# Kernel optimization log

Hardware: AMD Instinct MI355X
Metric: run time of the kernel (lower is better)

The kernel has to match this reference:

```python
import jax, jax.numpy as jnp
import numpy as np

D_MODEL = 256
NHEAD = 8
DK = D_MODEL // NHEAD
EDGE_FEAT_DIM = 7
N_NODES = 2048
N_EDGES = 65536
LN_EPS = 1e-5


def _ln(x, g, b):
    mu = jnp.mean(x, axis=-1, keepdims=True)
    var = jnp.mean(jnp.square(x - mu), axis=-1, keepdims=True)
    return (x - mu) * jax.lax.rsqrt(var + LN_EPS) * g + b


def setup_inputs() -> dict:
    key = jax.random.key(0)
    ks = jax.random.split(key, 16)
    d, h2 = D_MODEL, 2 * D_MODEL
    s = 0.02
    inp = {
        "h": jax.random.normal(ks[0], (N_NODES, d), jnp.float32),
        "edge_attr": jax.random.normal(ks[1], (N_EDGES, EDGE_FEAT_DIM), jnp.float32),
        # weights stored as (in, out): y = x @ W + b (matches torch Linear math)
        "Wq": s * jax.random.normal(ks[2], (d, d), jnp.float32),
        "bq": jnp.zeros((d,), jnp.float32),
        "Wk": s * jax.random.normal(ks[3], (d, d), jnp.float32),
        "bk": jnp.zeros((d,), jnp.float32),
        "Wv": s * jax.random.normal(ks[4], (d, d), jnp.float32),
        "bv": jnp.zeros((d,), jnp.float32),
        "Wo": s * jax.random.normal(ks[5], (d, d), jnp.float32),
        "bo": jnp.zeros((d,), jnp.float32),
        "We": s * jax.random.normal(ks[6], (EDGE_FEAT_DIM, NHEAD), jnp.float32),
        "be": jnp.zeros((NHEAD,), jnp.float32),
        "ln1_g": jnp.ones((d,), jnp.float32),
        "ln1_b": jnp.zeros((d,), jnp.float32),
        "fln_g": jnp.ones((d,), jnp.float32),
        "fln_b": jnp.zeros((d,), jnp.float32),
        "W1": s * jax.random.normal(ks[7], (d, h2), jnp.float32),
        "b1": jnp.zeros((h2,), jnp.float32),
        "W2": s * jax.random.normal(ks[8], (h2, d), jnp.float32),
        "b2": jnp.zeros((d,), jnp.float32),
        "edge_index": jax.random.randint(ks[9], (2, N_EDGES), 0, N_NODES, jnp.int64 if jax.config.jax_enable_x64 else jnp.int32),
    }
    return inp


def reference(h, edge_attr, Wq, bq, Wk, bk, Wv, bv, Wo, bo, We, be,
              ln1_g, ln1_b, fln_g, fln_b, W1, b1, W2, b2, edge_index):
    N = h.shape[0]
    res = h
    # edge bias scattered into dense (N, N, H) tensor
    eb = edge_attr @ We + be                                  # (E, H)
    attn_bias = jnp.zeros((N, N, NHEAD), h.dtype).at[edge_index[0], edge_index[1]].set(eb)
    Q = (h @ Wq + bq).reshape(N, NHEAD, DK)
    K = (h @ Wk + bk).reshape(N, NHEAD, DK)
    V = (h @ Wv + bv).reshape(N, NHEAD, DK)
    scores = jnp.einsum('nhd,mhd->nmh', Q, K) / jnp.sqrt(jnp.float32(DK)) + attn_bias
    attn = jax.nn.softmax(scores, axis=1)                     # softmax over keys m
    out = jnp.einsum('nmh,mhd->nhd', attn, V).reshape(N, D_MODEL)
    out = out @ Wo + bo
    h1 = _ln(res + out, ln1_g, ln1_b)
    ffn = jax.nn.gelu(_ln(h1, fln_g, fln_b) @ W1 + b1, approximate=False) @ W2 + b2
    return h1 + ffn
```

## Files before the change

### kernel.cpp

```cpp
#include <hip/hip_runtime.h>
#include <math.h>

#define NN 2048
#define NE 65536
#define DM 256
#define NH 8
#define DKH 32
#define CAP 128
#define TM2 128
#define SPLIT 4

typedef __attribute__((ext_vector_type(8))) short bf16x8;
typedef __attribute__((ext_vector_type(4))) float f32x4;

#define WAVE_LDS_SYNC() __asm__ volatile("s_waitcnt lgkmcnt(0)" ::: "memory")

__device__ __forceinline__ unsigned short f2b(float f) {
    unsigned u = __float_as_uint(f);
    unsigned r = (u + 0x7FFFu + ((u >> 16) & 1u)) >> 16;
    return (unsigned short)r;
}
__device__ __forceinline__ float b2f(unsigned short s) {
    return __uint_as_float(((unsigned)s) << 16);
}
__device__ __forceinline__ unsigned pk2(float a, float b) {
    unsigned ua = __float_as_uint(a) + 0x8000u;
    unsigned ub = __float_as_uint(b) + 0x8000u;
    return (ua >> 16) | (ub & 0xFFFF0000u);
}

__global__ __launch_bounds__(256) void prep_all_kernel(
    const float* __restrict__ Wq, const float* __restrict__ Wk,
    const float* __restrict__ Wv, const float* __restrict__ Wo,
    const float* __restrict__ W1, const float* __restrict__ W2,
    const float* __restrict__ ea, const float* __restrict__ We,
    const float* __restrict__ be, const int* __restrict__ ei,
    unsigned short* __restrict__ Wqkvt, unsigned short* __restrict__ Wot,
    unsigned short* __restrict__ W1t, unsigned short* __restrict__ W2t,
    float* __restrict__ eb, int* __restrict__ cnt, int* __restrict__ lst)
{
    int b = blockIdx.x;
    if (b < 2048) {
        int i = b * 256 + threadIdx.x;
        if (i < 196608) {
            int n = i >> 8, k = i & 255;
            const float* W = (n < 256) ? Wq : (n < 512) ? Wk : Wv;
            Wqkvt[i] = f2b(W[k * 256 + (n & 255)]);
        } else if (i < 262144) {
            int j = i - 196608;
            int n = j >> 8, k = j & 255;
            Wot[j] = f2b(Wo[k * 256 + n]);
        } else if (i < 393216) {
            int j = i - 262144;
            int n = j >> 8, k = j & 255;
            W1t[j] = f2b(W1[(size_t)k * 512 + n]);
        } else {
            int j = i - 393216;
            int n = j >> 9, k = j & 511;
            W2t[j] = f2b(W2[(size_t)k * 256 + n]);
        }
    } else {
        int e = (b - 2048) * 256 + threadIdx.x;
        float acc[NH];
#pragma unroll
        for (int hh = 0; hh < NH; ++hh) acc[hh] = be[hh];
#pragma unroll
        for (int f = 0; f < 7; ++f) {
            float x = ea[e * 7 + f];
#pragma unroll
            for (int hh = 0; hh < NH; ++hh) acc[hh] = fmaf(x, We[f * NH + hh], acc[hh]);
        }
#pragma unroll
        for (int hh = 0; hh < NH; ++hh)
            eb[e * NH + hh] = acc[hh] * 1.44269504088896f;
        int s = ei[e];
        int p = atomicAdd(&cnt[s], 1);
        if (p < CAP) lst[s * CAP + p] = e;
    }
}

__global__ __launch_bounds__(128) void rowprep_kernel(
    const int* __restrict__ ei, const int* __restrict__ cnt,
    const int* __restrict__ lst, int* __restrict__ sortedDest,
    int* __restrict__ sortedE, int* __restrict__ rowOff)
{
    __shared__ int ds[CAP], es[CAP];
    __shared__ int bc[16], off[17];
    int n = blockIdx.x, t = threadIdx.x;
    int c = cnt[n]; if (c > CAP) c = CAP;
    if (t < 16) bc[t] = 0;
    int e = -1, d = -1;
    if (t < c) { e = lst[n * CAP + t]; d = ei[NE + e]; }
    ds[t] = d; es[t] = e;
    __syncthreads();
    bool win = (t < c);
    if (win) {
        for (int j = 0; j < c; ++j)
            if (ds[j] == d && es[j] > e) { win = false; break; }
    }
    int bkt = (d >= 0) ? (d >> 7) : 0;
    int pos = -1;
    if (win) pos = atomicAdd(&bc[bkt], 1);
    __syncthreads();
    if (t == 0) {
        int s = 0;
        for (int i = 0; i < 16; ++i) { off[i] = s; s += bc[i]; }
        off[16] = s;
    }
    __syncthreads();
    if (win) {
        int p = off[bkt] + pos;
        sortedDest[n * CAP + p] = d;
        sortedE[n * CAP + p] = e;
    }
    if (t < 17) rowOff[n * 17 + t] = off[t];
}

template <int EPI, int MT, int AF32>
__global__ __launch_bounds__(MT * 4) void gemm_bf16(
    const void* __restrict__ Av, const unsigned short* __restrict__ Bt,
    const float* __restrict__ bias0, const float* __restrict__ bias1,
    const float* __restrict__ bias2, const float* __restrict__ resid,
    void* __restrict__ out0, void* __restrict__ out1, void* __restrict__ out2,
    int M, int N, int K)
{
    __shared__ __align__(16) unsigned short As[MT][136];
    __shared__ __align__(16) unsigned short Bs[64][136];
    int tid = threadIdx.x;
    int wv = tid >> 6, l = tid & 63, l15 = l & 15, quad = l >> 4;
    int m0 = blockIdx.y * MT, n0 = blockIdx.x * 64;

    f32x4 acc[4];
#pragma unroll
    for (int i = 0; i < 4; ++i) acc[i] = (f32x4){0.f, 0.f, 0.f, 0.f};

    for (int k0 = 0; k0 < K; k0 += 128) {
        if (MT == 64) {
            int row = tid >> 2, cb = (tid & 3) * 32;
            if (AF32) {
                const float* ap = (const float*)Av + (size_t)(m0 + row) * K + k0 + cb;
#pragma unroll
                for (int i = 0; i < 4; ++i) {
                    float4 f0 = *(const float4*)(ap + i * 8);
                    float4 f1 = *(const float4*)(ap + i * 8 + 4);
                    uint4 pk = { pk2(f0.x, f0.y), pk2(f0.z, f0.w),
                                 pk2(f1.x, f1.y), pk2(f1.z, f1.w) };
                    *(uint4*)&As[row][cb + i * 8] = pk;
                }
            } else {
                const unsigned short* ap =
                    (const unsigned short*)Av + (size_t)(m0 + row) * K + k0 + cb;
#pragma unroll
                for (int i = 0; i < 4; ++i)
                    *(uint4*)&As[row][cb + i * 8] = *(const uint4*)(ap + i * 8);
            }
            const unsigned short* bp = Bt + (size_t)(n0 + row) * K + k0 + cb;
#pragma unroll
            for (int i = 0; i < 4; ++i)
                *(uint4*)&Bs[row][cb + i * 8] = *(const uint4*)(bp + i * 8);
        } else {
            int rowa = tid >> 2, cba = (tid & 3) * 32;
            const unsigned short* ap =
                (const unsigned short*)Av + (size_t)(m0 + rowa) * K + k0 + cba;
#pragma unroll
            for (int i = 0; i < 4; ++i)
                *(uint4*)&As[rowa][cba + i * 8] = *(const uint4*)(ap + i * 8);
            int rowb = tid >> 1, cbb = (tid & 1) * 64;
            const unsigned short* bp = Bt + (size_t)(n0 + rowb) * K + k0 + cbb;
#pragma unroll
            for (int i = 0; i < 8; ++i)
                *(uint4*)&Bs[rowb][cbb + i * 8] = *(const uint4*)(bp + i * 8);
        }
        __syncthreads();
#pragma unroll
        for (int ks = 0; ks < 4; ++ks) {
            bf16x8 a = *(const bf16x8*)&As[wv * 16 + l15][ks * 32 + quad * 8];
#pragma unroll
            for (int nt = 0; nt < 4; ++nt) {
                bf16x8 b = *(const bf16x8*)&Bs[nt * 16 + l15][ks * 32 + quad * 8];
                acc[nt] = __builtin_amdgcn_mfma_f32_16x16x32_bf16(a, b, acc[nt], 0, 0, 0);
            }
        }
        __syncthreads();
    }

#pragma unroll
    for (int nt = 0; nt < 4; ++nt) {
        int colb = n0 + nt * 16;
        if (EPI == 2 && colb >= 512) {
            int n = colb + l15 - 512;
            float bv = bias2[n];
            uint2 pk = { pk2(acc[nt][0] + bv, acc[nt][1] + bv),
                         pk2(acc[nt][2] + bv, acc[nt][3] + bv) };
            *(uint2*)((unsigned short*)out2 + (size_t)n * NN + m0 + wv * 16 + quad * 4) = pk;
            continue;
        }
#pragma unroll
        for (int r = 0; r < 4; ++r) {
            int row = m0 + wv * 16 + quad * 4 + r;
            int col = colb + l15;
            float v = acc[nt][r];
            if (EPI == 0) {
                v += bias0[col];
                if (resid) v += resid[(size_t)row * N + col];
                ((float*)out0)[(size_t)row * N + col] = v;
            } else if (EPI == 1) {
                v += bias0[col];
                v = 0.5f * v * (1.0f + erff(v * 0.70710678118654752f));
                ((unsigned short*)out0)[(size_t)row * N + col] = f2b(v);
            } else {
                if (col < 256) {
                    v = (v + bias0[col]) * 0.2550348592f;
                    ((unsigned short*)out0)[(size_t)row * 256 + col] = f2b(v);
                } else {
                    v += bias1[col - 256];
                    ((unsigned short*)out1)[(size_t)row * 256 + col - 256] = f2b(v);
                }
            }
        }
    }
}

__global__ __launch_bounds__(256) void attn_mfma(
    const unsigned short* __restrict__ Qb, const unsigned short* __restrict__ Kb,
    const unsigned short* __restrict__ Vt, const float* __restrict__ eb,
    const int* __restrict__ sortedDest, const int* __restrict__ sortedE,
    const int* __restrict__ rowOff,
    float* __restrict__ accD, float* __restrict__ lD)
{
    __shared__ __align__(16) unsigned short Ks[TM2][40];
    __shared__ __align__(16) unsigned short Vs[32][TM2 + 8];
    __shared__ __align__(16) unsigned short Pn[4][16][TM2 + 16];
    int h = blockIdx.y, tid = threadIdx.x;
    int wv = tid >> 6, l = tid & 63, l15 = l & 15, quad = l >> 4;
    int n0 = blockIdx.x * 64 + wv * 16;
    int mz = blockIdx.z;

    bf16x8 aq = *(const bf16x8*)(Qb + (size_t)(n0 + l15) * DM + h * 32 + quad * 8);

    f32x4 oacc[2];
    oacc[0] = (f32x4){0.f, 0.f, 0.f, 0.f};
    oacc[1] = (f32x4){0.f, 0.f, 0.f, 0.f};
    float lacc = 0.f;
    float dreg = 0.f;
    const unsigned short* Vth = Vt + (size_t)h * 32 * NN;

    int r16 = l >> 2, sub = l & 3;
    int frow = n0 + r16;

    for (int t = 0; t < NN / (TM2 * SPLIT); ++t) {
        int m0 = (mz * (NN / SPLIT)) + t * TM2;
        int ti = m0 >> 7;
        {
            int r = tid >> 1, kc = (tid & 1) * 16;
            const unsigned short* ks = Kb + (size_t)(m0 + r) * DM + h * 32 + kc;
            *(uint4*)&Ks[r][kc]     = *(const uint4*)(ks);
            *(uint4*)&Ks[r][kc + 8] = *(const uint4*)(ks + 8);
            int d = tid >> 3, mc = (tid & 7) * 16;
            const unsigned short* vs = Vth + (size_t)d * NN + m0 + mc;
            *(uint4*)&Vs[d][mc]     = *(const uint4*)(vs);
            *(uint4*)&Vs[d][mc + 8] = *(const uint4*)(vs + 8);
        }
        __syncthreads();
#pragma unroll
        for (int mt = 0; mt < TM2 / 16; ++mt) {
            bf16x8 ak = *(const bf16x8*)&Ks[mt * 16 + l15][quad * 8];
            f32x4 s = __builtin_amdgcn_mfma_f32_16x16x32_bf16(
                ak, aq, (f32x4){0.f, 0.f, 0.f, 0.f}, 0, 0, 0);
            float p0 = __builtin_amdgcn_exp2f(s[0]);
            float p1 = __builtin_amdgcn_exp2f(s[1]);
            float p2 = __builtin_amdgcn_exp2f(s[2]);
            float p3 = __builtin_amdgcn_exp2f(s[3]);
            lacc += (p0 + p1) + (p2 + p3);
            *(uint2*)&Pn[wv][l15][mt * 16 + quad * 4] =
                (uint2){pk2(p0, p1), pk2(p2, p3)};
        }
        WAVE_LDS_SYNC();
        {
            int o0 = rowOff[frow * 17 + ti];
            int o1 = rowOff[frow * 17 + ti + 1];
            for (int idx = o0 + sub; idx < o1; idx += 4) {
                int d = sortedDest[frow * CAP + idx] - m0;
                int e = sortedE[frow * CAP + idx];
                float expb = __builtin_amdgcn_exp2f(eb[e * NH + h]);
                float pold = b2f(Pn[wv][r16][d]);
                Pn[wv][r16][d] = f2b(pold * expb);
                dreg += pold * (expb - 1.0f);
            }
        }
        WAVE_LDS_SYNC();
#pragma unroll
        for (int kc = 0; kc < TM2 / 32; ++kc) {
            bf16x8 ap = *(const bf16x8*)&Pn[wv][l15][kc * 32 + quad * 8];
#pragma unroll
            for (int nt = 0; nt < 2; ++nt) {
                bf16x8 bv = *(const bf16x8*)&Vs[nt * 16 + l15][kc * 32 + quad * 8];
                oacc[nt] = __builtin_amdgcn_mfma_f32_16x16x32_bf16(ap, bv, oacc[nt], 0, 0, 0);
            }
        }
        __syncthreads();
    }

    lacc += __shfl_xor(lacc, 16);
    lacc += __shfl_xor(lacc, 32);
    dreg += __shfl_xor(dreg, 1);
    dreg += __shfl_xor(dreg, 2);
    float dtot = __shfl(dreg, l15 * 4);
    float* lDp = lD + (size_t)mz * NN * NH;
    if (l < 16)
        lDp[(size_t)(n0 + l) * NH + h] = lacc + dtot;
    float* aDp = accD + (size_t)mz * NN * DM;
#pragma unroll
    for (int nt = 0; nt < 2; ++nt)
#pragma unroll
        for (int r = 0; r < 4; ++r)
            aDp[(size_t)(n0 + quad * 4 + r) * DM + h * 32 + nt * 16 + l15] = oacc[nt][r];
}

__global__ __launch_bounds__(256) void wo_ln_kernel(
    const float* __restrict__ accD, const float* __restrict__ lD,
    const unsigned short* __restrict__ Wot, const float* __restrict__ bo,
    const float* __restrict__ h, const float* __restrict__ g1,
    const float* __restrict__ b1, const float* __restrict__ g2,
    const float* __restrict__ b2, float* __restrict__ H1,
    unsigned short* __restrict__ X2b)
{
    __shared__ float linv[16][8];
    __shared__ __align__(16) unsigned short As[16][264];
    __shared__ __align__(16) unsigned short Bs[256][40];
    __shared__ float Tt[16][264];
    __shared__ unsigned short X2s[16][264];
    int tid = threadIdx.x, m0 = blockIdx.x * 16;
    int wv = tid >> 6, l = tid & 63, l15 = l & 15, quad = l >> 4;

    if (tid < 128) {
        int r = tid >> 3, hh = tid & 7;
        float ls = 0.f;
#pragma unroll
        for (int s = 0; s < SPLIT; ++s)
            ls += lD[(size_t)s * NN * NH + (size_t)(m0 + r) * NH + hh];
        linv[r][hh] = 1.0f / ls;
    }
    __syncthreads();
#pragma unroll
    for (int ch = 0; ch < 16; ++ch) {
        float o = 0.f;
#pragma unroll
        for (int s = 0; s < SPLIT; ++s)
            o += accD[(size_t)s * NN * DM + (size_t)(m0 + ch) * DM + tid];
        As[ch][tid] = f2b(o * linv[ch][tid >> 5]);
    }
    __syncthreads();

    f32x4 acc[4];
#pragma unroll
    for (int i = 0; i < 4; ++i) acc[i] = (f32x4){0.f, 0.f, 0.f, 0.f};

    for (int k0 = 0; k0 < 256; k0 += 32) {
#pragma unroll
        for (int ps = 0; ps < 4; ++ps) {
            int row = ps * 64 + (tid >> 2), kk = (tid & 3) * 8;
            *(uint4*)&Bs[row][kk] = *(const uint4*)(Wot + (size_t)row * 256 + k0 + kk);
        }
        __syncthreads();
        bf16x8 a = *(const bf16x8*)&As[l15][k0 + quad * 8];
#pragma unroll
        for (int nt = 0; nt < 4; ++nt) {
            bf16x8 b = *(const bf16x8*)&Bs[wv * 64 + nt * 16 + l15][quad * 8];
            acc[nt] = __builtin_amdgcn_mfma_f32_16x16x32_bf16(a, b, acc[nt], 0, 0, 0);
        }
        __syncthreads();
    }

#pragma unroll
    for (int nt = 0; nt < 4; ++nt)
#pragma unroll
        for (int r = 0; r < 4; ++r) {
            int row = quad * 4 + r, col = wv * 64 + nt * 16 + l15;
            Tt[row][col] = acc[nt][r] + bo[col] + h[(size_t)(m0 + row) * DM + col];
        }
    __syncthreads();

    int rr = tid >> 4, l16 = tid & 15;
    float x[16];
#pragma unroll
    for (int j = 0; j < 16; ++j) x[j] = Tt[rr][l16 + 16 * j];
    float mu = 0.f;
#pragma unroll
    for (int j = 0; j < 16; ++j) mu += x[j];
#pragma unroll
    for (int off = 1; off < 16; off <<= 1) mu += __shfl_xor(mu, off);
    mu *= (1.0f / 256.0f);
    float var = 0.f;
#pragma unroll
    for (int j = 0; j < 16; ++j) { float d = x[j] - mu; var += d * d; }
#pragma unroll
    for (int off = 1; off < 16; off <<= 1) var += __shfl_xor(var, off);
    float rs = rsqrtf(var * (1.0f / 256.0f) + 1e-5f);
    float y[16]; float mu2 = 0.f;
#pragma unroll
    for (int j = 0; j < 16; ++j) {
        int c = l16 + 16 * j;
        y[j] = (x[j] - mu) * rs * g1[c] + b1[c];
        mu2 += y[j];
    }
#pragma unroll
    for (int off = 1; off < 16; off <<= 1) mu2 += __shfl_xor(mu2, off);
    mu2 *= (1.0f / 256.0f);
    float var2 = 0.f;
#pragma unroll
    for (int j = 0; j < 16; ++j) { float d = y[j] - mu2; var2 += d * d; }
#pragma unroll
    for (int off = 1; off < 16; off <<= 1) var2 += __shfl_xor(var2, off);
    float rs2 = rsqrtf(var2 * (1.0f / 256.0f) + 1e-5f);
#pragma unroll
    for (int j = 0; j < 16; ++j) {
        int c = l16 + 16 * j;
        Tt[rr][c] = y[j];
        X2s[rr][c] = f2b((y[j] - mu2) * rs2 * g2[c] + b2[c]);
    }
    __syncthreads();
#pragma unroll
    for (int ch = 0; ch < 16; ++ch) {
        H1[(size_t)(m0 + ch) * DM + tid] = Tt[ch][tid];
        X2b[(size_t)(m0 + ch) * DM + tid] = X2s[ch][tid];
    }
}

extern "C" void kernel_launch(void* const* d_in, const int* in_sizes, int n_in,
                              void* d_out, int out_size, void* d_ws, size_t ws_size,
                              hipStream_t stream)
{
    const float* h    = (const float*)d_in[0];
    const float* ea   = (const float*)d_in[1];
    const float* Wq   = (const float*)d_in[2];
    const float* bq   = (const float*)d_in[3];
    const float* Wk   = (const float*)d_in[4];
    const float* bk   = (const float*)d_in[5];
    const float* Wv   = (const float*)d_in[6];
    const float* bv   = (const float*)d_in[7];
    const float* Wo   = (const float*)d_in[8];
    const float* bo   = (const float*)d_in[9];
    const float* We   = (const float*)d_in[10];
    const float* be   = (const float*)d_in[11];
    const float* ln1g = (const float*)d_in[12];
    const float* ln1b = (const float*)d_in[13];
    const float* flng = (const float*)d_in[14];
    const float* flnb = (const float*)d_in[15];
    const float* W1   = (const float*)d_in[16];
    const float* b1   = (const float*)d_in[17];
    const float* W2   = (const float*)d_in[18];
    const float* b2   = (const float*)d_in[19];
    const int*   ei   = (const int*)d_in[20];
    float* out = (float*)d_out;

    char* p = (char*)d_ws;
    float* eb   = (float*)p;           p += (size_t)NE * NH * 4;
    int*   cnt  = (int*)p;             p += (size_t)NN * 4;
    int*   lst  = (int*)p;             p += (size_t)NN * CAP * 4;
    int*   sD   = (int*)p;             p += (size_t)NN * CAP * 4;
    int*   sE   = (int*)p;             p += (size_t)NN * CAP * 4;
    int*   rOff = (int*)p;             p += (size_t)NN * 17 * 4;
    unsigned short* Wqkvt = (unsigned short*)p; p += (size_t)768 * 256 * 2;
    unsigned short* Wot   = (unsigned short*)p; p += (size_t)256 * 256 * 2;
    unsigned short* W1t   = (unsigned short*)p; p += (size_t)512 * 256 * 2;
    unsigned short* W2t   = (unsigned short*)p; p += (size_t)256 * 512 * 2;
    unsigned short* Qb    = (unsigned short*)p; p += (size_t)NN * DM * 2;
    unsigned short* Kb    = (unsigned short*)p; p += (size_t)NN * DM * 2;
    unsigned short* Vt    = (unsigned short*)p; p += (size_t)NN * DM * 2;
    float* accD = (float*)p;           p += (size_t)SPLIT * NN * DM * 4;
    float* lD   = (float*)p;           p += (size_t)SPLIT * NN * NH * 4;
    float* H1   = (float*)p;           p += (size_t)NN * DM * 4;
    unsigned short* X2b   = (unsigned short*)p; p += (size_t)NN * DM * 2;
    unsigned short* F1b   = (unsigned short*)p; p += (size_t)NN * 512 * 2;

    hipMemsetAsync(cnt, 0, (size_t)NN * 4, stream);
    prep_all_kernel<<<2048 + NE / 256, 256, 0, stream>>>(
        Wq, Wk, Wv, Wo, W1, W2, ea, We, be, ei,
        Wqkvt, Wot, W1t, W2t, eb, cnt, lst);
    rowprep_kernel<<<NN, 128, 0, stream>>>(ei, cnt, lst, sD, sE, rOff);

    gemm_bf16<2, 64, 1><<<dim3(768 / 64, NN / 64), 256, 0, stream>>>(
        h, Wqkvt, bq, bk, bv, nullptr, Qb, Kb, Vt, NN, 768, 256);

    attn_mfma<<<dim3(NN / 64, NH, SPLIT), 256, 0, stream>>>(
        Qb, Kb, Vt, eb, sD, sE, rOff, accD, lD);

    wo_ln_kernel<<<NN / 16, 256, 0, stream>>>(
        accD, lD, Wot, bo, h, ln1g, ln1b, flng, flnb, H1, X2b);

    gemm_bf16<1, 64, 0><<<dim3(512 / 64, NN / 64), 256, 0, stream>>>(
        X2b, W1t, b1, nullptr, nullptr, nullptr, F1b, nullptr, nullptr, NN, 512, 256);
    gemm_bf16<0, 32, 0><<<dim3(256 / 64, NN / 32), 128, 0, stream>>>(
        F1b, W2t, b2, nullptr, nullptr, H1, out, nullptr, nullptr, NN, 256, 512);
}
```

Before: 173.3 us.

## Fuse Wo projection, layernorms and both FFN GEMMs into one tail kernel

Merges the Wo+LN kernel with the two FFN GEMMs into a single kernel per 16-row block. H1, normalized X2 and GELU activations stay in shared memory rather than round-tripping through global buffers, and two launches go away. The cost is that each block reloads the full W1 and W2 weights from global/L2 with only 128 blocks, and each GEMM uses a single 16-row MFMA tile. Occupancy drops from the larger LDS footprint, so the FFN GEMMs may lose parallelism compared with the separate tiled kernels.

```diff
diff --git a/kernel.cpp b/kernel.cpp
--- a/kernel.cpp
+++ b/kernel.cpp
@@ -317,19 +317,22 @@
             aDp[(size_t)(n0 + quad * 4 + r) * DM + h * 32 + nt * 16 + l15] = oacc[nt][r];
 }
 
-__global__ __launch_bounds__(256) void wo_ln_kernel(
+__global__ __launch_bounds__(256) void tail_fused_kernel(
     const float* __restrict__ accD, const float* __restrict__ lD,
     const unsigned short* __restrict__ Wot, const float* __restrict__ bo,
-    const float* __restrict__ h, const float* __restrict__ g1,
-    const float* __restrict__ b1, const float* __restrict__ g2,
-    const float* __restrict__ b2, float* __restrict__ H1,
-    unsigned short* __restrict__ X2b)
+    const float* __restrict__ h, const float* __restrict__ ln1g,
+    const float* __restrict__ ln1b, const float* __restrict__ flng,
+    const float* __restrict__ flnb,
+    const unsigned short* __restrict__ W1t, const float* __restrict__ fb1,
+    const unsigned short* __restrict__ W2t, const float* __restrict__ fb2,
+    float* __restrict__ out)
 {
     __shared__ float linv[16][8];
     __shared__ __align__(16) unsigned short As[16][264];
-    __shared__ __align__(16) unsigned short Bs[256][40];
+    __shared__ __align__(16) unsigned short Wfs[512][40];
     __shared__ float Tt[16][264];
-    __shared__ unsigned short X2s[16][264];
+    __shared__ __align__(16) unsigned short X2s[16][264];
+    __shared__ __align__(16) unsigned short F1s[16][520];
     int tid = threadIdx.x, m0 = blockIdx.x * 16;
     int wv = tid >> 6, l = tid & 63, l15 = l & 15, quad = l >> 4;
 
@@ -360,13 +363,13 @@
 #pragma unroll
         for (int ps = 0; ps < 4; ++ps) {
             int row = ps * 64 + (tid >> 2), kk = (tid & 3) * 8;
-            *(uint4*)&Bs[row][kk] = *(const uint4*)(Wot + (size_t)row * 256 + k0 + kk);
+            *(uint4*)&Wfs[row][kk] = *(const uint4*)(Wot + (size_t)row * 256 + k0 + kk);
         }
         __syncthreads();
         bf16x8 a = *(const bf16x8*)&As[l15][k0 + quad * 8];
 #pragma unroll
         for (int nt = 0; nt < 4; ++nt) {
-            bf16x8 b = *(const bf16x8*)&Bs[wv * 64 + nt * 16 + l15][quad * 8];
+            bf16x8 b = *(const bf16x8*)&Wfs[wv * 64 + nt * 16 + l15][quad * 8];
             acc[nt] = __builtin_amdgcn_mfma_f32_16x16x32_bf16(a, b, acc[nt], 0, 0, 0);
         }
         __syncthreads();
@@ -401,7 +404,7 @@
 #pragma unroll
     for (int j = 0; j < 16; ++j) {
         int c = l16 + 16 * j;
-        y[j] = (x[j] - mu) * rs * g1[c] + b1[c];
+        y[j] = (x[j] - mu) * rs * ln1g[c] + ln1b[c];
         mu2 += y[j];
     }
 #pragma unroll
@@ -417,14 +420,65 @@
     for (int j = 0; j < 16; ++j) {
         int c = l16 + 16 * j;
         Tt[rr][c] = y[j];
-        X2s[rr][c] = f2b((y[j] - mu2) * rs2 * g2[c] + b2[c]);
-    }
-    __syncthreads();
-#pragma unroll
-    for (int ch = 0; ch < 16; ++ch) {
-        H1[(size_t)(m0 + ch) * DM + tid] = Tt[ch][tid];
-        X2b[(size_t)(m0 + ch) * DM + tid] = X2s[ch][tid];
-    }
+        X2s[rr][c] = f2b((y[j] - mu2) * rs2 * flng[c] + flnb[c]);
+    }
+    __syncthreads();
+
+    f32x4 acc1[8];
+#pragma unroll
+    for (int i = 0; i < 8; ++i) acc1[i] = (f32x4){0.f, 0.f, 0.f, 0.f};
+
+    for (int k0 = 0; k0 < 256; k0 += 32) {
+#pragma unroll
+        for (int ps = 0; ps < 8; ++ps) {
+            int row = ps * 64 + (tid >> 2), kk = (tid & 3) * 8;
+            *(uint4*)&Wfs[row][kk] = *(const uint4*)(W1t + (size_t)row * 256 + k0 + kk);
+        }
+        __syncthreads();
+        bf16x8 a = *(const bf16x8*)&X2s[l15][k0 + quad * 8];
+#pragma unroll
+        for (int nt = 0; nt < 8; ++nt) {
+            bf16x8 b = *(const bf16x8*)&Wfs[wv * 128 + nt * 16 + l15][quad * 8];
+            acc1[nt] = __builtin_amdgcn_mfma_f32_16x16x32_bf16(a, b, acc1[nt], 0, 0, 0);
+        }
+        __syncthreads();
+    }
+#pragma unroll
+    for (int nt = 0; nt < 8; ++nt)
+#pragma unroll
+        for (int r = 0; r < 4; ++r) {
+            int row = quad * 4 + r, col = wv * 128 + nt * 16 + l15;
+            float v = acc1[nt][r] + fb1[col];
+            v = 0.5f * v * (1.0f + erff(v * 0.70710678118654752f));
+            F1s[row][col] = f2b(v);
+        }
+
+    f32x4 acc2[4];
+#pragma unroll
+    for (int i = 0; i < 4; ++i) acc2[i] = (f32x4){0.f, 0.f, 0.f, 0.f};
+
+    for (int k0 = 0; k0 < 512; k0 += 32) {
+#pragma unroll
+        for (int ps = 0; ps < 4; ++ps) {
+            int row = ps * 64 + (tid >> 2), kk = (tid & 3) * 8;
+            *(uint4*)&Wfs[row][kk] = *(const uint4*)(W2t + (size_t)row * 512 + k0 + kk);
+        }
+        __syncthreads();
+        bf16x8 a = *(const bf16x8*)&F1s[l15][k0 + quad * 8];
+#pragma unroll
+        for (int nt = 0; nt < 4; ++nt) {
+            bf16x8 b = *(const bf16x8*)&Wfs[wv * 64 + nt * 16 + l15][quad * 8];
+            acc2[nt] = __builtin_amdgcn_mfma_f32_16x16x32_bf16(a, b, acc2[nt], 0, 0, 0);
+        }
+        __syncthreads();
+    }
+#pragma unroll
+    for (int nt = 0; nt < 4; ++nt)
+#pragma unroll
+        for (int r = 0; r < 4; ++r) {
+            int row = quad * 4 + r, col = wv * 64 + nt * 16 + l15;
+            out[(size_t)(m0 + row) * DM + col] = acc2[nt][r] + fb2[col] + Tt[row][col];
+        }
 }
 
 extern "C" void kernel_launch(void* const* d_in, const int* in_sizes, int n_in,
@@ -470,9 +524,6 @@
     unsigned short* Vt    = (unsigned short*)p; p += (size_t)NN * DM * 2;
     float* accD = (float*)p;           p += (size_t)SPLIT * NN * DM * 4;
     float* lD   = (float*)p;           p += (size_t)SPLIT * NN * NH * 4;
-    float* H1   = (float*)p;           p += (size_t)NN * DM * 4;
-    unsigned short* X2b   = (unsigned short*)p; p += (size_t)NN * DM * 2;
-    unsigned short* F1b   = (unsigned short*)p; p += (size_t)NN * 512 * 2;
 
     hipMemsetAsync(cnt, 0, (size_t)NN * 4, stream);
     prep_all_kernel<<<2048 + NE / 256, 256, 0, stream>>>(
@@ -486,11 +537,7 @@
     attn_mfma<<<dim3(NN / 64, NH, SPLIT), 256, 0, stream>>>(
         Qb, Kb, Vt, eb, sD, sE, rOff, accD, lD);
 
-    wo_ln_kernel<<<NN / 16, 256, 0, stream>>>(
-        accD, lD, Wot, bo, h, ln1g, ln1b, flng, flnb, H1, X2b);
-
-    gemm_bf16<1, 64, 0><<<dim3(512 / 64, NN / 64), 256, 0, stream>>>(
-        X2b, W1t, b1, nullptr, nullptr, nullptr, F1b, nullptr, nullptr, NN, 512, 256);
-    gemm_bf16<0, 32, 0><<<dim3(256 / 64, NN / 32), 128, 0, stream>>>(
-        F1b, W2t, b2, nullptr, nullptr, H1, out, nullptr, nullptr, NN, 256, 512);
-}
+    tail_fused_kernel<<<NN / 16, 256, 0, stream>>>(
+        accD, lD, Wot, bo, h, ln1g, ln1b, flng, flnb,
+        W1t, b1, W2t, b2, out);
+}
```

After: 172.8 us. Within noise of the previous version (-0.3%).
